# Kernel optimization log

Hardware: AMD Instinct MI355X
Metric: run time of the kernel (lower is better)

## Reference

```python
import jax, jax.numpy as jnp
import numpy as np

H = 256   # node_hidden_dim == edge_hidden_dim

def _ln(x, g, b):
    m = x.mean(-1, keepdims=True)
    v = ((x - m) ** 2).mean(-1, keepdims=True)
    return (x - m) / jnp.sqrt(v + 1e-5) * g + b

def _slnn(x, W, b, g, beta):
    # Linear -> LayerNorm -> ReLU (SingleLayerNN)
    return jax.nn.relu(_ln(x @ W.T + b, g, beta))

def _gru_mean(x, Wih, Whh, bih, bhh):
    # x: [E, T, Din]; torch GRU gate order (r, z, n); returns mean over time of outputs [E, H]
    h0 = jnp.zeros((x.shape[0], Whh.shape[1]), x.dtype)
    def step(h, xt):
        gi = xt @ Wih.T + bih
        gh = h @ Whh.T + bhh
        ir, iz, inn = jnp.split(gi, 3, axis=-1)
        hr, hz, hn = jnp.split(gh, 3, axis=-1)
        r = jax.nn.sigmoid(ir + hr)
        z = jax.nn.sigmoid(iz + hz)
        n = jnp.tanh(inn + r * hn)
        h_new = (1.0 - z) * n + z * h
        return h_new, h_new
    _, ys = jax.lax.scan(step, h0, jnp.swapaxes(x, 0, 1))  # [T, E, H]
    return ys.mean(axis=0)

def setup_inputs() -> dict:
    key = jax.random.key(0)
    ks = iter(jax.random.split(key, 64))
    rn = lambda shape, s=1.0: (jax.random.normal(next(ks), shape, jnp.float32) * s)
    ru = lambda shape: jax.random.uniform(next(ks), shape, jnp.float32)
    ri = lambda shape, hi: jax.random.randint(next(ks), shape, 0, hi, jnp.int32)
    N0, N1, N2, E0, E1, T = 40000, 10000, 2000, 100000, 20000, 8
    Dn, De, FC, C = 128, 64, 512, 16
    inp = {
        'node_features': rn((N0, Dn)),
        'edge_features_0': rn((E0, T, De)),
        'edge_features_1': rn((E1, T, H)),
        'history_0': rn((N0, H)),
        'history_1': rn((N1, H)),
        'agg_history_1': rn((N2, H)),
        'subg_norm_1': ru((N1, 1)),
        'subg_norm_2': ru((N2, 1)),
        'norm_2': ru((N2, 1)),
        'src0': ri((E0,), N0), 'dst0': ri((E0,), N1),
        'src1': ri((E1,), N1), 'dst1': ri((E1,), N2),
        'self_nid0': ri((N1,), N0), 'self_nid1': ri((N2,), N1),
        # parameters
        'gru0_Wih': rn((3 * H, De), 0.05), 'gru0_Whh': rn((3 * H, H), 0.05),
        'gru0_bih': rn((3 * H,), 0.05), 'gru0_bhh': rn((3 * H,), 0.05),
        'gru1_Wih': rn((3 * H, H), 0.05), 'gru1_Whh': rn((3 * H, H), 0.05),
        'gru1_bih': rn((3 * H,), 0.05), 'gru1_bhh': rn((3 * H,), 0.05),
        'phi0_W': rn((H, Dn + H), 0.05), 'phi0_b': rn((H,), 0.05),
        'phi0_g': jnp.ones((H,)), 'phi0_beta': jnp.zeros((H,)),
        'phi1_W': rn((H, 2 * H), 0.05), 'phi1_b': rn((H,), 0.05),
        'phi1_g': jnp.ones((H,)), 'phi1_beta': jnp.zeros((H,)),
        'nu0_W': rn((H, 2 * H), 0.05), 'nu0_b': rn((H,), 0.05),
        'nu0_g': jnp.ones((H,)), 'nu0_beta': jnp.zeros((H,)),
        'nu1_W': rn((H, 2 * H), 0.05), 'nu1_b': rn((H,), 0.05),
        'nu1_g': jnp.ones((H,)), 'nu1_beta': jnp.zeros((H,)),
        'fc1_W': rn((FC, H), 0.05), 'fc1_b': rn((FC,), 0.05),
        'fc2_W': rn((C, FC), 0.05), 'fc2_b': rn((C,), 0.05),
    }
    return inp

def reference(node_features, edge_features_0, edge_features_1, history_0, history_1,
              agg_history_1, subg_norm_1, subg_norm_2, norm_2,
              gru0_Wih, gru0_Whh, gru0_bih, gru0_bhh,
              gru1_Wih, gru1_Whh, gru1_bih, gru1_bhh,
              phi0_W, phi0_b, phi0_g, phi0_beta,
              phi1_W, phi1_b, phi1_g, phi1_beta,
              nu0_W, nu0_b, nu0_g, nu0_beta,
              nu1_W, nu1_b, nu1_g, nu1_beta,
              fc1_W, fc1_b, fc2_W, fc2_b,
              src0, dst0, src1, dst1, self_nid0, self_nid1):
    N1, N2 = self_nid0.shape[0], self_nid1.shape[0]
    # ---- layer 0 ----
    self_h0 = _slnn(jnp.concatenate([jnp.zeros((N1, H), node_features.dtype),
                                     node_features[self_nid0]], 1),
                    phi0_W, phi0_b, phi0_g, phi0_beta)                       # [N1, H]
    edge_emb0 = _gru_mean(edge_features_0, gru0_Wih, gru0_Whh, gru0_bih, gru0_bhh)  # [E0, H]
    nb0 = _slnn(jnp.concatenate([node_features[src0], edge_emb0], 1),
                phi0_W, phi0_b, phi0_g, phi0_beta)
    msg0 = jax.nn.relu(nb0 - history_0[src0])
    delta_nb0 = jax.ops.segment_sum(msg0, dst0, num_segments=N1)             # scatter-sum
    new_h0 = (delta_nb0 - self_h0) * subg_norm_1
    h1 = _slnn(jnp.concatenate([new_h0, self_h0], 1), nu0_W, nu0_b, nu0_g, nu0_beta)  # [N1, H]
    # ---- layer 1 ----
    self_h1 = _slnn(jnp.concatenate([jnp.zeros((N2, H), h1.dtype), h1[self_nid1]], 1),
                    phi1_W, phi1_b, phi1_g, phi1_beta)                       # [N2, H]
    self_delta_h1 = self_h1 - history_1[self_nid1]
    edge_emb1 = _gru_mean(edge_features_1, gru1_Wih, gru1_Whh, gru1_bih, gru1_bhh)  # [E1, H]
    nb1 = _slnn(jnp.concatenate([h1[src1], edge_emb1], 1),
                phi1_W, phi1_b, phi1_g, phi1_beta)
    msg1 = jax.nn.relu(nb1 - history_1[src1])
    delta_nb1 = jax.ops.segment_sum(msg1, dst1, num_segments=N2)
    new_h1 = (delta_nb1 - self_delta_h1) * subg_norm_2 + agg_history_1 * norm_2
    h2 = _slnn(jnp.concatenate([new_h1, self_h1], 1), nu1_W, nu1_b, nu1_g, nu1_beta)  # [N2, H]
    # ---- readout (no activation between fc1 and fc2, as in source) ----
    logit = (h2 @ fc1_W.T + fc1_b) @ fc2_W.T + fc2_b
    return logit
```

## Files before the change

kernel.cpp:

```cpp
#include <hip/hip_runtime.h>

typedef unsigned short u16;
typedef __attribute__((ext_vector_type(4))) float f32x4;
typedef __attribute__((ext_vector_type(8))) short bf16x8;
#define MFMA16(a,b,c) __builtin_amdgcn_mfma_f32_16x16x32_bf16((a),(b),(c),0,0,0)

template<int N> struct ic { static constexpr int v = N; };

__device__ __forceinline__ u16 f2bf(float f){
  unsigned int u = __float_as_uint(f);
  u += 0x7FFFu + ((u >> 16) & 1u);
  return (u16)(u >> 16);
}
__device__ __forceinline__ float bf2f(u16 h){
  return __uint_as_float(((unsigned int)h) << 16);
}
__device__ __forceinline__ float sigmoid_f(float x){
  x = fminf(fmaxf(x, -30.f), 30.f);
  return __fdividef(1.f, 1.f + __expf(-x));
}
__device__ __forceinline__ float tanh_f(float x){
  x = fminf(fmaxf(x, -15.f), 15.f);
  float e = __expf(-2.f * x);
  return __fdividef(1.f - e, 1.f + e);
}

__global__ void cvt_bf16_kernel(const float* __restrict__ in, u16* __restrict__ out, int n){
  int i = blockIdx.x * 256 + threadIdx.x;
  int stride = gridDim.x * 256;
  for (; i < n; i += stride) out[i] = f2bf(in[i]);
}

template<int R>
__device__ __forceinline__ void ln_stats_rows(const float* __restrict__ O,
                                              float* __restrict__ mean_s,
                                              float* __restrict__ rstd_s){
  const int tid  = threadIdx.x;
  const int wave = tid >> 6, lane = tid & 63;
  constexpr int RW = R / 4;
  #pragma unroll
  for (int rr = 0; rr < RW; rr++){
    const int r = wave * RW + rr;
    float s = 0.f, q = 0.f;
    #pragma unroll
    for (int i = lane; i < 256; i += 64){ float v = O[r*256 + i]; s += v; q += v*v; }
    #pragma unroll
    for (int off = 32; off; off >>= 1){ s += __shfl_down(s, off); q += __shfl_down(q, off); }
    if (lane == 0){
      float m   = s * (1.f/256.f);
      float var = q * (1.f/256.f) - m*m;
      mean_s[r] = m;
      rstd_s[r] = rsqrtf(fmaxf(var, 0.f) + 1e-5f);
    }
  }
}

template<int TM, int DIN, int NFD, int XBUFS>
__global__ __launch_bounds__(512, 2)
void gru_mfma_kernel(int E,
    const float* __restrict__ x,
    const float* __restrict__ nodef,
    const int*   __restrict__ src,
    const int*   __restrict__ dst,
    const float* __restrict__ hist,
    const u16*   __restrict__ Wih,
    const u16*   __restrict__ Whh,
    const float* __restrict__ bih,
    const float* __restrict__ bhh,
    const u16*   __restrict__ phiW,
    const float* __restrict__ phib,
    const float* __restrict__ phig,
    const float* __restrict__ phibeta,
    float* __restrict__ delta)
{
  constexpr int HP   = 264;
  constexpr int XP   = DIN + 8;
  constexpr int NP   = NFD + 8;
  constexpr int KP   = NFD + 256;
  constexpr int MT   = TM / 16;
  constexpr int NF4  = (TM * DIN) / 2048;
  constexpr int HBUF = TM * HP;
  constexpr int XBUF = TM * XP;

  __shared__ __align__(16) u16 hb[2 * HBUF];
  __shared__ __align__(16) u16 xb[XBUFS * XBUF];
  __shared__ int srcs_s[TM], dsts_s[TM];

  const int tid  = threadIdx.x;
  const int wave = tid >> 6, lane = tid & 63;
  const int quad = lane >> 4, ln15 = lane & 15;
  const int qoff = quad * 8;
  const int cbase = wave * 32;
  const int e0   = blockIdx.x * TM;

  if (tid < TM){
    int e  = e0 + tid;
    int ec = (e < E) ? e : (E - 1);
    srcs_s[tid] = src[ec];
    dsts_s[tid] = dst[ec];
  }

  int cn[2]; float brc[2], bzc[2], bnic[2], bnhc[2], pb[2], gg[2], gb[2];
  #pragma unroll
  for (int nt = 0; nt < 2; nt++){
    int c   = cbase + nt * 16 + ln15;
    cn[nt]  = c;
    brc[nt]  = bih[c]       + bhh[c];
    bzc[nt]  = bih[256 + c] + bhh[256 + c];
    bnic[nt] = bih[512 + c];
    bnhc[nt] = bhh[512 + c];
    pb[nt]   = phib[c];
    gg[nt]   = phig[c];
    gb[nt]   = phibeta[c];
  }

  #pragma unroll
  for (int j = 0; j < NF4; j++){
    int i4 = tid + j * 512;
    int e  = i4 / (DIN / 4);
    int k4 = (i4 % (DIN / 4)) * 4;
    int ge = (e0 + e < E) ? (e0 + e) : (E - 1);
    float4 v = *(const float4*)(x + (size_t)ge * (8 * DIN) + k4);
    ushort4 u;
    u.x = f2bf(v.x); u.y = f2bf(v.y); u.z = f2bf(v.z); u.w = f2bf(v.w);
    *(ushort4*)(xb + e * XP + k4) = u;
  }
  __syncthreads();

  float hs[2][MT][4];
  #pragma unroll
  for (int nt = 0; nt < 2; nt++)
    #pragma unroll
    for (int mt = 0; mt < MT; mt++)
      #pragma unroll
      for (int q = 0; q < 4; q++) hs[nt][mt][q] = 0.f;

  const f32x4 zero4 = {0.f, 0.f, 0.f, 0.f};

  #pragma unroll 1
  for (int t = 0; t < 8; t++){
    const u16* rd = hb + ((t & 1) ^ 1) * HBUF;
    u16*       wr = hb + (t & 1) * HBUF;
    const u16* xr = xb + ((XBUFS == 2) ? (t & 1) * XBUF : 0);

    float4 xpre[NF4];
    if (t < 7){
      #pragma unroll
      for (int j = 0; j < NF4; j++){
        int i4 = tid + j * 512;
        int e  = i4 / (DIN / 4);
        int k4 = (i4 % (DIN / 4)) * 4;
        int ge = (e0 + e < E) ? (e0 + e) : (E - 1);
        xpre[j] = *(const float4*)(x + (size_t)ge * (8 * DIN) + (size_t)(t + 1) * DIN + k4);
      }
    }

    auto phase = [&](auto ntc){
      constexpr int NT = decltype(ntc)::v;
      const int c = cn[NT];
      f32x4 aR[MT], aZ[MT], aNI[MT], aNH[MT];
      #pragma unroll
      for (int mt = 0; mt < MT; mt++){
        aR[mt] = zero4; aZ[mt] = zero4; aNI[mt] = zero4; aNH[mt] = zero4;
      }
      if (t > 0){
        #pragma unroll
        for (int kt = 0; kt < 8; kt++){
          bf16x8 a[MT];
          #pragma unroll
          for (int mt = 0; mt < MT; mt++)
            a[mt] = *(const bf16x8*)(rd + (mt*16 + ln15) * HP + kt * 32 + qoff);
          const u16* bp = Whh + (size_t)c * 256 + kt * 32 + qoff;
          bf16x8 br = *(const bf16x8*)(bp);
          bf16x8 bz = *(const bf16x8*)(bp + 256 * 256);
          bf16x8 bn = *(const bf16x8*)(bp + 512 * 256);
          #pragma unroll
          for (int mt = 0; mt < MT; mt++){
            aR[mt]  = MFMA16(a[mt], br, aR[mt]);
            aZ[mt]  = MFMA16(a[mt], bz, aZ[mt]);
            aNH[mt] = MFMA16(a[mt], bn, aNH[mt]);
          }
        }
      }
      #pragma unroll
      for (int kt = 0; kt < DIN / 32; kt++){
        bf16x8 a[MT];
        #pragma unroll
        for (int mt = 0; mt < MT; mt++)
          a[mt] = *(const bf16x8*)(xr + (mt*16 + ln15) * XP + kt * 32 + qoff);
        const u16* bp = Wih + (size_t)c * DIN + kt * 32 + qoff;
        bf16x8 br = *(const bf16x8*)(bp);
        bf16x8 bz = *(const bf16x8*)(bp + 256 * DIN);
        bf16x8 bn = *(const bf16x8*)(bp + 512 * DIN);
        #pragma unroll
        for (int mt = 0; mt < MT; mt++){
          aR[mt]  = MFMA16(a[mt], br, aR[mt]);
          aZ[mt]  = MFMA16(a[mt], bz, aZ[mt]);
          aNI[mt] = MFMA16(a[mt], bn, aNI[mt]);
        }
      }
      #pragma unroll
      for (int mt = 0; mt < MT; mt++){
        #pragma unroll
        for (int q = 0; q < 4; q++){
          const int e = mt * 16 + quad * 4 + q;
          float r = sigmoid_f(aR[mt][q] + brc[NT]);
          float z = sigmoid_f(aZ[mt][q] + bzc[NT]);
          float n = tanh_f(aNI[mt][q] + bnic[NT] + r * (aNH[mt][q] + bnhc[NT]));
          float hold = (t > 0) ? bf2f(rd[e * HP + c]) : 0.f;
          float hnew = (1.f - z) * n + z * hold;
          hs[NT][mt][q] += hnew;
          if (t < 7) wr[e * HP + c] = f2bf(hnew);
        }
      }
    };
    phase(ic<0>());
    phase(ic<1>());

    if (XBUFS == 1){
      __syncthreads();
      if (t < 7){
        #pragma unroll
        for (int j = 0; j < NF4; j++){
          int i4 = tid + j * 512;
          int e  = i4 / (DIN / 4);
          int k4 = (i4 % (DIN / 4)) * 4;
          ushort4 u;
          u.x = f2bf(xpre[j].x); u.y = f2bf(xpre[j].y);
          u.z = f2bf(xpre[j].z); u.w = f2bf(xpre[j].w);
          *(ushort4*)(xb + e * XP + k4) = u;
        }
        __syncthreads();
      }
    } else {
      if (t < 7){
        u16* xw = xb + (((t + 1) & 1)) * XBUF;
        #pragma unroll
        for (int j = 0; j < NF4; j++){
          int i4 = tid + j * 512;
          int e  = i4 / (DIN / 4);
          int k4 = (i4 % (DIN / 4)) * 4;
          ushort4 u;
          u.x = f2bf(xpre[j].x); u.y = f2bf(xpre[j].y);
          u.z = f2bf(xpre[j].z); u.w = f2bf(xpre[j].w);
          *(ushort4*)(xw + e * XP + k4) = u;
        }
      }
      __syncthreads();
    }
  }

  u16* nb = (XBUFS == 1) ? (hb + HBUF) : xb;
  {
    u16* eb = hb;
    #pragma unroll
    for (int nt = 0; nt < 2; nt++)
      #pragma unroll
      for (int mt = 0; mt < MT; mt++)
        #pragma unroll
        for (int q = 0; q < 4; q++){
          const int e = mt * 16 + quad * 4 + q;
          eb[e * HP + cn[nt]] = f2bf(hs[nt][mt][q] * 0.125f);
        }
    constexpr int R4 = NFD / 4;
    for (int i = tid; i < TM * R4; i += 512){
      int e  = i / R4;
      int k4 = (i - e * R4) * 4;
      const float4 v = *(const float4*)(nodef + (size_t)srcs_s[e] * NFD + k4);
      ushort4 u;
      u.x = f2bf(v.x); u.y = f2bf(v.y); u.z = f2bf(v.z); u.w = f2bf(v.w);
      *(ushort4*)(nb + e * NP + k4) = u;
    }
  }
  __syncthreads();

  f32x4 P[2][MT];
  #pragma unroll
  for (int nt = 0; nt < 2; nt++)
    #pragma unroll
    for (int mt = 0; mt < MT; mt++) P[nt][mt] = zero4;

  #pragma unroll
  for (int kt = 0; kt < NFD / 32; kt++){
    bf16x8 a[MT];
    #pragma unroll
    for (int mt = 0; mt < MT; mt++)
      a[mt] = *(const bf16x8*)(nb + (mt*16 + ln15) * NP + kt * 32 + qoff);
    #pragma unroll
    for (int nt = 0; nt < 2; nt++){
      const u16* bp = phiW + (size_t)cn[nt] * KP + kt * 32 + qoff;
      bf16x8 b = *(const bf16x8*)(bp);
      #pragma unroll
      for (int mt = 0; mt < MT; mt++) P[nt][mt] = MFMA16(a[mt], b, P[nt][mt]);
    }
  }
  #pragma unroll
  for (int kt = 0; kt < 8; kt++){
    bf16x8 a[MT];
    #pragma unroll
    for (int mt = 0; mt < MT; mt++)
      a[mt] = *(const bf16x8*)(hb + (mt*16 + ln15) * HP + kt * 32 + qoff);
    #pragma unroll
    for (int nt = 0; nt < 2; nt++){
      const u16* bp = phiW + (size_t)cn[nt] * KP + NFD + kt * 32 + qoff;
      bf16x8 b = *(const bf16x8*)(bp);
      #pragma unroll
      for (int mt = 0; mt < MT; mt++) P[nt][mt] = MFMA16(a[mt], b, P[nt][mt]);
    }
  }

  float* sums_s = (float*)((XBUFS == 1) ? (void*)xb : (void*)(hb + HBUF));
  float* sqs_s  = sums_s + 8 * TM;
  float* mean_s = sqs_s  + 8 * TM;
  float* rstd_s = mean_s + TM;

  float sl[MT][4], sq_[MT][4];
  #pragma unroll
  for (int mt = 0; mt < MT; mt++)
    #pragma unroll
    for (int q = 0; q < 4; q++){
      float v0 = P[0][mt][q] + pb[0];
      float v1 = P[1][mt][q] + pb[1];
      P[0][mt][q] = v0; P[1][mt][q] = v1;
      sl[mt][q]  = v0 + v1;
      sq_[mt][q] = v0 * v0 + v1 * v1;
    }
  #pragma unroll
  for (int off = 1; off < 16; off <<= 1){
    #pragma unroll
    for (int mt = 0; mt < MT; mt++)
      #pragma unroll
      for (int q = 0; q < 4; q++){
        sl[mt][q]  += __shfl_xor(sl[mt][q], off);
        sq_[mt][q] += __shfl_xor(sq_[mt][q], off);
      }
  }
  if (ln15 == 0){
    #pragma unroll
    for (int mt = 0; mt < MT; mt++)
      #pragma unroll
      for (int q = 0; q < 4; q++){
        int row = mt * 16 + quad * 4 + q;
        sums_s[wave * TM + row] = sl[mt][q];
        sqs_s[wave * TM + row]  = sq_[mt][q];
      }
  }
  __syncthreads();
  if (tid < TM){
    float m = 0.f, qq = 0.f;
    #pragma unroll
    for (int w = 0; w < 8; w++){ m += sums_s[w * TM + tid]; qq += sqs_s[w * TM + tid]; }
    m  *= (1.f / 256.f);
    qq *= (1.f / 256.f);
    mean_s[tid] = m;
    rstd_s[tid] = rsqrtf(fmaxf(qq - m * m, 0.f) + 1e-5f);
  }
  __syncthreads();

  #pragma unroll
  for (int nt = 0; nt < 2; nt++){
    const int c = cn[nt];
    #pragma unroll
    for (int mt = 0; mt < MT; mt++)
      #pragma unroll
      for (int q = 0; q < 4; q++){
        const int e  = mt * 16 + quad * 4 + q;
        const int ge = e0 + e;
        float y = (P[nt][mt][q] - mean_s[e]) * rstd_s[e] * gg[nt] + gb[nt];
        y = fmaxf(y, 0.f);
        float mv = y - hist[(size_t)srcs_s[e] * 256 + c];
        if (ge < E && mv > 0.f)
          atomicAdd(delta + (size_t)dsts_s[e] * 256 + c, mv);
      }
  }
}

template<int K, int WS>
__global__ __launch_bounds__(256)
void self_slnn_kernel(int N,
    const float* __restrict__ feat,
    const int*   __restrict__ nid,
    const float* __restrict__ W,
    const float* __restrict__ b,
    const float* __restrict__ g,
    const float* __restrict__ beta,
    const float* __restrict__ hist,
    float* __restrict__ out,
    float* __restrict__ out2)
{
  constexpr int R = 8;
  __shared__ float X[R*K];
  __shared__ float O[R*256];
  __shared__ float mean_s[R], rstd_s[R];
  __shared__ int   nids[R];
  const int tid = threadIdx.x;
  const int n0  = blockIdx.x * R;
  if (tid < R) nids[tid] = (n0 + tid < N) ? nid[n0 + tid] : 0;
  __syncthreads();
  for (int i = tid; i < R*K; i += 256){
    int r = i / K, k = i - r*K;
    X[i] = feat[(size_t)nids[r]*K + k];
  }
  __syncthreads();
  const int c = tid;
  const float* Wc = W + (size_t)c*WS + (WS - K);
  float acc[R];
  const float bc0 = b[c];
  #pragma unroll
  for (int r = 0; r < R; r++) acc[r] = bc0;
  #pragma unroll 1
  for (int k = 0; k < K; k += 4){
    float4 w = *(const float4*)(Wc + k);
    #pragma unroll
    for (int r = 0; r < R; r++){
      float4 xv = *(const float4*)(X + r*K + k);
      acc[r] += w.x*xv.x + w.y*xv.y + w.z*xv.z + w.w*xv.w;
    }
  }
  #pragma unroll
  for (int r = 0; r < R; r++) O[r*256 + c] = acc[r];
  __syncthreads();
  ln_stats_rows<R>(O, mean_s, rstd_s);
  __syncthreads();
  const float gc = g[c], bc = beta[c];
  #pragma unroll
  for (int r = 0; r < R; r++){
    int n = n0 + r;
    if (n < N){
      float y = fmaxf((acc[r] - mean_s[r]) * rstd_s[r] * gc + bc, 0.f);
      out[(size_t)n*256 + c] = y;
      if (out2) out2[(size_t)n*256 + c] = y - hist[(size_t)nids[r]*256 + c];
    }
  }
}

__global__ __launch_bounds__(256)
void compose_slnn_kernel(int N,
    const float* __restrict__ delta,
    const float* __restrict__ selfA,
    const float* __restrict__ selfB,
    const float* __restrict__ subg,
    const float* __restrict__ agg,
    const float* __restrict__ normv,
    const float* __restrict__ W,
    const float* __restrict__ b,
    const float* __restrict__ g,
    const float* __restrict__ beta,
    float* __restrict__ out)
{
  constexpr int R = 8;
  __shared__ float X[R*512];
  __shared__ float O[R*256];
  __shared__ float mean_s[R], rstd_s[R];
  const int tid = threadIdx.x;
  const int n0  = blockIdx.x * R;
  for (int i = tid; i < R*512; i += 256){
    int r = i >> 9, k = i & 511;
    int n = n0 + r;
    float v = 0.f;
    if (n < N){
      if (k < 256){
        v = (delta[(size_t)n*256 + k] - selfA[(size_t)n*256 + k]) * subg[n];
        if (agg) v += agg[(size_t)n*256 + k] * normv[n];
      } else {
        v = selfB[(size_t)n*256 + (k - 256)];
      }
    }
    X[i] = v;
  }
  __syncthreads();
  const int c = tid;
  const float* Wc = W + (size_t)c*512;
  float acc[R];
  const float bc0 = b[c];
  #pragma unroll
  for (int r = 0; r < R; r++) acc[r] = bc0;
  #pragma unroll 1
  for (int k = 0; k < 512; k += 4){
    float4 w = *(const float4*)(Wc + k);
    #pragma unroll
    for (int r = 0; r < R; r++){
      float4 xv = *(const float4*)(X + r*512 + k);
      acc[r] += w.x*xv.x + w.y*xv.y + w.z*xv.z + w.w*xv.w;
    }
  }
  #pragma unroll
  for (int r = 0; r < R; r++) O[r*256 + c] = acc[r];
  __syncthreads();
  ln_stats_rows<R>(O, mean_s, rstd_s);
  __syncthreads();
  const float gc = g[c], bc = beta[c];
  #pragma unroll
  for (int r = 0; r < R; r++){
    int n = n0 + r;
    if (n < N)
      out[(size_t)n*256 + c] = fmaxf((acc[r] - mean_s[r]) * rstd_s[r] * gc + bc, 0.f);
  }
}

__global__ __launch_bounds__(256)
void readout_kernel(int N,
    const float* __restrict__ h2,
    const float* __restrict__ W1,
    const float* __restrict__ b1,
    const float* __restrict__ W2,
    const float* __restrict__ b2,
    float* __restrict__ out)
{
  constexpr int R = 8;
  __shared__ float X[R*256];
  __shared__ float T[R*512];
  const int tid = threadIdx.x;
  const int n0  = blockIdx.x * R;
  for (int i = tid; i < R*256; i += 256){
    int r = i >> 8, k = i & 255;
    int n = n0 + r;
    X[i] = (n < N) ? h2[(size_t)n*256 + k] : 0.f;
  }
  __syncthreads();
  const int c = tid;
  const float* Wa = W1 + (size_t)c*256;
  const float* Wb = W1 + (size_t)(c+256)*256;
  float acca[R], accb[R];
  const float ba = b1[c], bb = b1[c+256];
  #pragma unroll
  for (int r = 0; r < R; r++){ acca[r] = ba; accb[r] = bb; }
  #pragma unroll 1
  for (int k = 0; k < 256; k += 4){
    float4 wa = *(const float4*)(Wa + k);
    float4 wb = *(const float4*)(Wb + k);
    #pragma unroll
    for (int r = 0; r < R; r++){
      float4 xv = *(const float4*)(X + r*256 + k);
      acca[r] += wa.x*xv.x + wa.y*xv.y + wa.z*xv.z + wa.w*xv.w;
      accb[r] += wb.x*xv.x + wb.y*xv.y + wb.z*xv.z + wb.w*xv.w;
    }
  }
  #pragma unroll
  for (int r = 0; r < R; r++){ T[r*512 + c] = acca[r]; T[r*512 + 256 + c] = accb[r]; }
  __syncthreads();
  if (tid < R*16){
    int r = tid >> 4, o = tid & 15;
    int n = n0 + r;
    if (n < N){
      float s = b2[o];
      const float* w  = W2 + (size_t)o*512;
      const float* tr = T + r*512;
      #pragma unroll 4
      for (int k = 0; k < 512; k++) s += tr[k]*w[k];
      out[(size_t)n*16 + o] = s;
    }
  }
}

extern "C" void kernel_launch(void* const* d_in, const int* in_sizes, int n_in,
                              void* d_out, int out_size, void* d_ws, size_t ws_size,
                              hipStream_t stream) {
  const float* nf     = (const float*)d_in[0];
  const float* x0     = (const float*)d_in[1];
  const float* x1     = (const float*)d_in[2];
  const float* hist0  = (const float*)d_in[3];
  const float* hist1  = (const float*)d_in[4];
  const float* aggh1  = (const float*)d_in[5];
  const float* subg1  = (const float*)d_in[6];
  const float* subg2  = (const float*)d_in[7];
  const float* norm2  = (const float*)d_in[8];
  const int*   src0   = (const int*)d_in[9];
  const int*   dst0   = (const int*)d_in[10];
  const int*   src1   = (const int*)d_in[11];
  const int*   dst1   = (const int*)d_in[12];
  const int*   nid0   = (const int*)d_in[13];
  const int*   nid1   = (const int*)d_in[14];
  const float* g0Wih  = (const float*)d_in[15];
  const float* g0Whh  = (const float*)d_in[16];
  const float* g0bih  = (const float*)d_in[17];
  const float* g0bhh  = (const float*)d_in[18];
  const float* g1Wih  = (const float*)d_in[19];
  const float* g1Whh  = (const float*)d_in[20];
  const float* g1bih  = (const float*)d_in[21];
  const float* g1bhh  = (const float*)d_in[22];
  const float* phi0W  = (const float*)d_in[23];
  const float* phi0b  = (const float*)d_in[24];
  const float* phi0g  = (const float*)d_in[25];
  const float* phi0be = (const float*)d_in[26];
  const float* phi1W  = (const float*)d_in[27];
  const float* phi1b  = (const float*)d_in[28];
  const float* phi1g  = (const float*)d_in[29];
  const float* phi1be = (const float*)d_in[30];
  const float* nu0W   = (const float*)d_in[31];
  const float* nu0b   = (const float*)d_in[32];
  const float* nu0g   = (const float*)d_in[33];
  const float* nu0be  = (const float*)d_in[34];
  const float* nu1W   = (const float*)d_in[35];
  const float* nu1b   = (const float*)d_in[36];
  const float* nu1g   = (const float*)d_in[37];
  const float* nu1be  = (const float*)d_in[38];
  const float* fc1W   = (const float*)d_in[39];
  const float* fc1b   = (const float*)d_in[40];
  const float* fc2W   = (const float*)d_in[41];
  const float* fc2b   = (const float*)d_in[42];

  const int E0 = in_sizes[9];
  const int E1 = in_sizes[11];
  const int N1 = in_sizes[13];
  const int N2 = in_sizes[14];

  float* ws     = (float*)d_ws;
  float* delta0 = ws;
  float* selfh0 = delta0 + (size_t)N1*256;
  float* h1p    = selfh0 + (size_t)N1*256;
  float* delta1 = h1p    + (size_t)N1*256;
  float* selfh1 = delta1 + (size_t)N2*256;
  float* selfd1 = selfh1 + (size_t)N2*256;
  float* h2p    = selfd1 + (size_t)N2*256;

  u16* wbf       = (u16*)(h2p + (size_t)N2*256);
  u16* g0Wih_bf  = wbf;
  u16* g0Whh_bf  = g0Wih_bf + 768*64;
  u16* phi0W_bf  = g0Whh_bf + 768*256;
  u16* g1Wih_bf  = phi0W_bf + 256*384;
  u16* g1Whh_bf  = g1Wih_bf + 768*256;
  u16* phi1W_bf  = g1Whh_bf + 768*256;

  hipMemsetAsync(delta0, 0, (size_t)N1*256*sizeof(float), stream);
  hipMemsetAsync(delta1, 0, (size_t)N2*256*sizeof(float), stream);

  cvt_bf16_kernel<<<192, 256, 0, stream>>>(g0Wih, g0Wih_bf, 768*64);
  cvt_bf16_kernel<<<768, 256, 0, stream>>>(g0Whh, g0Whh_bf, 768*256);
  cvt_bf16_kernel<<<384, 256, 0, stream>>>(phi0W, phi0W_bf, 256*384);
  cvt_bf16_kernel<<<768, 256, 0, stream>>>(g1Wih, g1Wih_bf, 768*256);
  cvt_bf16_kernel<<<768, 256, 0, stream>>>(g1Whh, g1Whh_bf, 768*256);
  cvt_bf16_kernel<<<512, 256, 0, stream>>>(phi1W, phi1W_bf, 256*512);

  const int gN1 = (N1 + 7) / 8;
  const int gN2 = (N2 + 7) / 8;

  self_slnn_kernel<128, 384><<<gN1, 256, 0, stream>>>(
      N1, nf, nid0, phi0W, phi0b, phi0g, phi0be, nullptr, selfh0, nullptr);

  gru_mfma_kernel<64, 64, 128, 1><<<(E0 + 63) / 64, 512, 0, stream>>>(
      E0, x0, nf, src0, dst0, hist0,
      g0Wih_bf, g0Whh_bf, g0bih, g0bhh,
      phi0W_bf, phi0b, phi0g, phi0be, delta0);

  compose_slnn_kernel<<<gN1, 256, 0, stream>>>(
      N1, delta0, selfh0, selfh0, subg1, nullptr, nullptr,
      nu0W, nu0b, nu0g, nu0be, h1p);

  self_slnn_kernel<256, 512><<<gN2, 256, 0, stream>>>(
      N2, h1p, nid1, phi1W, phi1b, phi1g, phi1be, hist1, selfh1, selfd1);

  gru_mfma_kernel<32, 256, 256, 2><<<(E1 + 31) / 32, 512, 0, stream>>>(
      E1, x1, h1p, src1, dst1, hist1,
      g1Wih_bf, g1Whh_bf, g1bih, g1bhh,
      phi1W_bf, phi1b, phi1g, phi1be, delta1);

  compose_slnn_kernel<<<gN2, 256, 0, stream>>>(
      N2, delta1, selfd1, selfh1, subg2, aggh1, norm2,
      nu1W, nu1b, nu1g, nu1be, h2p);

  readout_kernel<<<gN2, 256, 0, stream>>>(
      N2, h2p, fc1W, fc1b, fc2W, fc2b, (float*)d_out);

  (void)n_in; (void)out_size; (void)ws_size;
}
```

Before: 2.800 ms.

## Shrink GRU blocks to four waves with four column phases each

The fused GRU+phi kernel now runs 256-thread blocks, and each wave covers 64 hidden columns in four 16-column phases instead of 32 columns in two. Layer 0 drops its edge tile from 64 to 32 and gets more blocks. The double-buffered x path is removed: when there are too many float4s per thread, the next step's x is loaded straight from global after the step instead of being prefetched into registers. The aim is higher occupancy and less LDS per block, at the cost of more accumulator registers per thread and less overlap of the x load for layer 1.

New measurement: 3.981 ms. 1.42x slower.

```diff
diff --git a/kernel.cpp b/kernel.cpp
--- a/kernel.cpp
+++ b/kernel.cpp
@@ -55,8 +55,8 @@
   }
 }
 
-template<int TM, int DIN, int NFD, int XBUFS>
-__global__ __launch_bounds__(512, 2)
+template<int TM, int DIN, int NFD>
+__global__ __launch_bounds__(256, 4)
 void gru_mfma_kernel(int E,
     const float* __restrict__ x,
     const float* __restrict__ nodef,
@@ -78,19 +78,20 @@
   constexpr int NP   = NFD + 8;
   constexpr int KP   = NFD + 256;
   constexpr int MT   = TM / 16;
-  constexpr int NF4  = (TM * DIN) / 2048;
+  constexpr int NPH  = 4;
+  constexpr int NF4  = (TM * DIN) / 1024;
+  constexpr bool PRE = (NF4 <= 4);
   constexpr int HBUF = TM * HP;
-  constexpr int XBUF = TM * XP;
 
   __shared__ __align__(16) u16 hb[2 * HBUF];
-  __shared__ __align__(16) u16 xb[XBUFS * XBUF];
+  __shared__ __align__(16) u16 xb[TM * XP];
   __shared__ int srcs_s[TM], dsts_s[TM];
 
   const int tid  = threadIdx.x;
   const int wave = tid >> 6, lane = tid & 63;
   const int quad = lane >> 4, ln15 = lane & 15;
   const int qoff = quad * 8;
-  const int cbase = wave * 32;
+  const int cbase = wave * 64;
   const int e0   = blockIdx.x * TM;
 
   if (tid < TM){
@@ -100,23 +101,20 @@
     dsts_s[tid] = dst[ec];
   }
 
-  int cn[2]; float brc[2], bzc[2], bnic[2], bnhc[2], pb[2], gg[2], gb[2];
-  #pragma unroll
-  for (int nt = 0; nt < 2; nt++){
-    int c   = cbase + nt * 16 + ln15;
-    cn[nt]  = c;
+  int cn[NPH]; float brc[NPH], bzc[NPH], bnic[NPH], bnhc[NPH];
+  #pragma unroll
+  for (int nt = 0; nt < NPH; nt++){
+    int c    = cbase + nt * 16 + ln15;
+    cn[nt]   = c;
     brc[nt]  = bih[c]       + bhh[c];
     bzc[nt]  = bih[256 + c] + bhh[256 + c];
     bnic[nt] = bih[512 + c];
     bnhc[nt] = bhh[512 + c];
-    pb[nt]   = phib[c];
-    gg[nt]   = phig[c];
-    gb[nt]   = phibeta[c];
   }
 
   #pragma unroll
   for (int j = 0; j < NF4; j++){
-    int i4 = tid + j * 512;
+    int i4 = tid + j * 256;
     int e  = i4 / (DIN / 4);
     int k4 = (i4 % (DIN / 4)) * 4;
     int ge = (e0 + e < E) ? (e0 + e) : (E - 1);
@@ -127,9 +125,9 @@
   }
   __syncthreads();
 
-  float hs[2][MT][4];
-  #pragma unroll
-  for (int nt = 0; nt < 2; nt++)
+  float hs[NPH][MT][4];
+  #pragma unroll
+  for (int nt = 0; nt < NPH; nt++)
     #pragma unroll
     for (int mt = 0; mt < MT; mt++)
       #pragma unroll
@@ -141,13 +139,12 @@
   for (int t = 0; t < 8; t++){
     const u16* rd = hb + ((t & 1) ^ 1) * HBUF;
     u16*       wr = hb + (t & 1) * HBUF;
-    const u16* xr = xb + ((XBUFS == 2) ? (t & 1) * XBUF : 0);
 
     float4 xpre[NF4];
-    if (t < 7){
+    if (PRE && t < 7){
       #pragma unroll
       for (int j = 0; j < NF4; j++){
-        int i4 = tid + j * 512;
+        int i4 = tid + j * 256;
         int e  = i4 / (DIN / 4);
         int k4 = (i4 % (DIN / 4)) * 4;
         int ge = (e0 + e < E) ? (e0 + e) : (E - 1);
@@ -187,7 +184,7 @@
         bf16x8 a[MT];
         #pragma unroll
         for (int mt = 0; mt < MT; mt++)
-          a[mt] = *(const bf16x8*)(xr + (mt*16 + ln15) * XP + kt * 32 + qoff);
+          a[mt] = *(const bf16x8*)(xb + (mt*16 + ln15) * XP + kt * 32 + qoff);
         const u16* bp = Wih + (size_t)c * DIN + kt * 32 + qoff;
         bf16x8 br = *(const bf16x8*)(bp);
         bf16x8 bz = *(const bf16x8*)(bp + 256 * DIN);
@@ -216,13 +213,15 @@
     };
     phase(ic<0>());
     phase(ic<1>());
-
-    if (XBUFS == 1){
-      __syncthreads();
-      if (t < 7){
+    phase(ic<2>());
+    phase(ic<3>());
+
+    __syncthreads();
+    if (t < 7){
+      if (PRE){
         #pragma unroll
         for (int j = 0; j < NF4; j++){
-          int i4 = tid + j * 512;
+          int i4 = tid + j * 256;
           int e  = i4 / (DIN / 4);
           int k4 = (i4 % (DIN / 4)) * 4;
           ushort4 u;
@@ -230,31 +229,28 @@
           u.z = f2bf(xpre[j].z); u.w = f2bf(xpre[j].w);
           *(ushort4*)(xb + e * XP + k4) = u;
         }
-        __syncthreads();
-      }
-    } else {
-      if (t < 7){
-        u16* xw = xb + (((t + 1) & 1)) * XBUF;
+      } else {
         #pragma unroll
         for (int j = 0; j < NF4; j++){
-          int i4 = tid + j * 512;
+          int i4 = tid + j * 256;
           int e  = i4 / (DIN / 4);
           int k4 = (i4 % (DIN / 4)) * 4;
+          int ge = (e0 + e < E) ? (e0 + e) : (E - 1);
+          float4 v = *(const float4*)(x + (size_t)ge * (8 * DIN) + (size_t)(t + 1) * DIN + k4);
           ushort4 u;
-          u.x = f2bf(xpre[j].x); u.y = f2bf(xpre[j].y);
-          u.z = f2bf(xpre[j].z); u.w = f2bf(xpre[j].w);
-          *(ushort4*)(xw + e * XP + k4) = u;
+          u.x = f2bf(v.x); u.y = f2bf(v.y); u.z = f2bf(v.z); u.w = f2bf(v.w);
+          *(ushort4*)(xb + e * XP + k4) = u;
         }
       }
       __syncthreads();
     }
   }
 
-  u16* nb = (XBUFS == 1) ? (hb + HBUF) : xb;
+  u16* nb = hb + HBUF;
   {
     u16* eb = hb;
     #pragma unroll
-    for (int nt = 0; nt < 2; nt++)
+    for (int nt = 0; nt < NPH; nt++)
       #pragma unroll
       for (int mt = 0; mt < MT; mt++)
         #pragma unroll
@@ -263,7 +259,7 @@
           eb[e * HP + cn[nt]] = f2bf(hs[nt][mt][q] * 0.125f);
         }
     constexpr int R4 = NFD / 4;
-    for (int i = tid; i < TM * R4; i += 512){
+    for (int i = tid; i < TM * R4; i += 256){
       int e  = i / R4;
       int k4 = (i - e * R4) * 4;
       const float4 v = *(const float4*)(nodef + (size_t)srcs_s[e] * NFD + k4);
@@ -274,9 +270,9 @@
   }
   __syncthreads();
 
-  f32x4 P[2][MT];
-  #pragma unroll
-  for (int nt = 0; nt < 2; nt++)
+  f32x4 P[NPH][MT];
+  #pragma unroll
+  for (int nt = 0; nt < NPH; nt++)
     #pragma unroll
     for (int mt = 0; mt < MT; mt++) P[nt][mt] = zero4;
 
@@ -287,7 +283,7 @@
     for (int mt = 0; mt < MT; mt++)
       a[mt] = *(const bf16x8*)(nb + (mt*16 + ln15) * NP + kt * 32 + qoff);
     #pragma unroll
-    for (int nt = 0; nt < 2; nt++){
+    for (int nt = 0; nt < NPH; nt++){
       const u16* bp = phiW + (size_t)cn[nt] * KP + kt * 32 + qoff;
       bf16x8 b = *(const bf16x8*)(bp);
       #pragma unroll
@@ -301,7 +297,7 @@
     for (int mt = 0; mt < MT; mt++)
       a[mt] = *(const bf16x8*)(hb + (mt*16 + ln15) * HP + kt * 32 + qoff);
     #pragma unroll
-    for (int nt = 0; nt < 2; nt++){
+    for (int nt = 0; nt < NPH; nt++){
       const u16* bp = phiW + (size_t)cn[nt] * KP + NFD + kt * 32 + qoff;
       bf16x8 b = *(const bf16x8*)(bp);
       #pragma unroll
@@ -309,22 +305,35 @@
     }
   }
 
-  float* sums_s = (float*)((XBUFS == 1) ? (void*)xb : (void*)(hb + HBUF));
-  float* sqs_s  = sums_s + 8 * TM;
-  float* mean_s = sqs_s  + 8 * TM;
+  float pb[NPH], gg[NPH], gb[NPH];
+  #pragma unroll
+  for (int nt = 0; nt < NPH; nt++){
+    pb[nt] = phib[cn[nt]];
+    gg[nt] = phig[cn[nt]];
+    gb[nt] = phibeta[cn[nt]];
+  }
+
+  float* sums_s = (float*)xb;
+  float* sqs_s  = sums_s + 4 * TM;
+  float* mean_s = sqs_s  + 4 * TM;
   float* rstd_s = mean_s + TM;
 
   float sl[MT][4], sq_[MT][4];
   #pragma unroll
   for (int mt = 0; mt < MT; mt++)
     #pragma unroll
-    for (int q = 0; q < 4; q++){
-      float v0 = P[0][mt][q] + pb[0];
-      float v1 = P[1][mt][q] + pb[1];
-      P[0][mt][q] = v0; P[1][mt][q] = v1;
-      sl[mt][q]  = v0 + v1;
-      sq_[mt][q] = v0 * v0 + v1 * v1;
-    }
+    for (int q = 0; q < 4; q++){ sl[mt][q] = 0.f; sq_[mt][q] = 0.f; }
+  #pragma unroll
+  for (int nt = 0; nt < NPH; nt++)
+    #pragma unroll
+    for (int mt = 0; mt < MT; mt++)
+      #pragma unroll
+      for (int q = 0; q < 4; q++){
+        float v = P[nt][mt][q] + pb[nt];
+        P[nt][mt][q] = v;
+        sl[mt][q]  += v;
+        sq_[mt][q] += v * v;
+      }
   #pragma unroll
   for (int off = 1; off < 16; off <<= 1){
     #pragma unroll
@@ -349,7 +358,7 @@
   if (tid < TM){
     float m = 0.f, qq = 0.f;
     #pragma unroll
-    for (int w = 0; w < 8; w++){ m += sums_s[w * TM + tid]; qq += sqs_s[w * TM + tid]; }
+    for (int w = 0; w < 4; w++){ m += sums_s[w * TM + tid]; qq += sqs_s[w * TM + tid]; }
     m  *= (1.f / 256.f);
     qq *= (1.f / 256.f);
     mean_s[tid] = m;
@@ -358,7 +367,7 @@
   __syncthreads();
 
   #pragma unroll
-  for (int nt = 0; nt < 2; nt++){
+  for (int nt = 0; nt < NPH; nt++){
     const int c = cn[nt];
     #pragma unroll
     for (int mt = 0; mt < MT; mt++)
@@ -638,7 +647,7 @@
   self_slnn_kernel<128, 384><<<gN1, 256, 0, stream>>>(
       N1, nf, nid0, phi0W, phi0b, phi0g, phi0be, nullptr, selfh0, nullptr);
 
-  gru_mfma_kernel<64, 64, 128, 1><<<(E0 + 63) / 64, 512, 0, stream>>>(
+  gru_mfma_kernel<32, 64, 128><<<(E0 + 31) / 32, 256, 0, stream>>>(
       E0, x0, nf, src0, dst0, hist0,
       g0Wih_bf, g0Whh_bf, g0bih, g0bhh,
       phi0W_bf, phi0b, phi0g, phi0be, delta0);
@@ -650,7 +659,7 @@
   self_slnn_kernel<256, 512><<<gN2, 256, 0, stream>>>(
       N2, h1p, nid1, phi1W, phi1b, phi1g, phi1be, hist1, selfh1, selfd1);
 
-  gru_mfma_kernel<32, 256, 256, 2><<<(E1 + 31) / 32, 512, 0, stream>>>(
+  gru_mfma_kernel<32, 256, 256><<<(E1 + 31) / 32, 256, 0, stream>>>(
       E1, x1, h1p, src1, dst1, hist1,
       g1Wih_bf, g1Whh_bf, g1bih, g1bhh,
       phi1W_bf, phi1b, phi1g, phi1be, delta1);
```
